# Kernel optimization log

Measured on AMD Instinct MI355X. Metric: run time of the kernel, lower is better.

The kernel has to match this reference:

```python
import jax, jax.numpy as jnp
import numpy as np

N_NODES = 100000
IN_CH = 256
OUT_CH = 128
N_EDGES = 3200000
SCALING_FACTOR = 1.8


def gcn_propagate(x, edge_index, num_nodes):
    """APPNP(K=1, alpha=0) == one step of D^-1/2 (A+I) D^-1/2 @ x."""
    row, col = edge_index[0], edge_index[1]
    loops = jnp.arange(num_nodes, dtype=edge_index.dtype)
    row = jnp.concatenate([row, loops])
    col = jnp.concatenate([col, loops])
    ones = jnp.ones(row.shape[0], dtype=x.dtype)
    deg = jax.ops.segment_sum(ones, col, num_segments=num_nodes)  # [N]
    dinv = jnp.where(deg > 0, jax.lax.rsqrt(deg), 0.0)
    norm = dinv[row] * dinv[col]  # [E+N]
    msgs = x[row] * norm[:, None]  # gather + scale, [E+N, C]
    return jax.ops.segment_sum(msgs, col, num_segments=num_nodes)  # [N, C]


def setup_inputs() -> dict:
    key = jax.random.key(0)
    ks = jax.random.split(key, 7)
    x = jax.random.normal(ks[0], (N_NODES, IN_CH), dtype=jnp.float32)
    edge_index = jax.random.randint(ks[1], (2, N_EDGES), 0, N_NODES, dtype=jnp.int64)
    s1 = 1.0 / np.sqrt(IN_CH)
    W1 = jax.random.uniform(ks[2], (IN_CH, OUT_CH), jnp.float32, -s1, s1)
    b1 = jax.random.uniform(ks[3], (OUT_CH,), jnp.float32, -s1, s1)
    W2 = jax.random.uniform(ks[4], (IN_CH, OUT_CH), jnp.float32, -s1, s1)
    b2 = jax.random.uniform(ks[5], (OUT_CH,), jnp.float32, -s1, s1)
    return {"x": x, "edge_index": edge_index, "W1": W1, "b1": b1, "W2": W2, "b2": b2}


def reference(x, edge_index, W1, b1, W2, b2):
    num_nodes = x.shape[0]
    # branch 1: linear1 then propagate
    x_ = x @ W1 + b1
    x_ = gcn_propagate(x_, edge_index, num_nodes)
    # branch 2: linear2, L2 normalize per-row, scale, then propagate
    h = x @ W2 + b2
    nrm = jnp.sqrt(jnp.sum(h * h, axis=1, keepdims=True))
    h = h / jnp.maximum(nrm, 1e-12) * SCALING_FACTOR
    h = gcn_propagate(h, edge_index, num_nodes)
    return (h, x_)
```

## Files before the change

kernel.cpp:

```cpp
#include <hip/hip_runtime.h>

#define IN_CH   256
#define OUT_CH  128
#define SCALE   1.8f
#define GT_M    64
#define BKT_SH  8
#define BKT_CAP 9216

using bf16x8 = __attribute__((ext_vector_type(8))) short;
using f32x4  = __attribute__((ext_vector_type(4))) float;

__device__ __forceinline__ float blo(unsigned int w) { return __uint_as_float(w << 16); }
__device__ __forceinline__ float bhi(unsigned int w) { return __uint_as_float(w & 0xffff0000u); }
__device__ __forceinline__ unsigned short f2b(float f) {
    unsigned int u = __float_as_uint(f);
    u += 0x7fffu + ((u >> 16) & 1u);
    return (unsigned short)(u >> 16);
}
__device__ __forceinline__ void split2(float f, unsigned short& h, unsigned short& l) {
    h = f2b(f);
    float hf = __uint_as_float((unsigned int)h << 16);
    l = f2b(f - hf);
}

__global__ __launch_bounds__(256) void wsplit_kernel(const float* __restrict__ W1, const float* __restrict__ b1,
                                                     const float* __restrict__ W2, const float* __restrict__ b2,
                                                     unsigned short* __restrict__ Wfh, unsigned short* __restrict__ Wfl,
                                                     float* __restrict__ bc, int* __restrict__ bktCur) {
    int n = blockIdx.x;
    int k = threadIdx.x;
    if (n < 2) {
        int i = n * 256 + k;
        bktCur[i] = i * BKT_CAP;
    }
    float w = (n < OUT_CH) ? W2[k * OUT_CH + n] : W1[k * OUT_CH + (n - OUT_CH)];
    unsigned short h, l;
    split2(w, h, l);
    int idx = (((k >> 5) * 16 + (n >> 4)) * 64 + ((k >> 3) & 3) * 16 + (n & 15)) * 8 + (k & 7);
    Wfh[idx] = h;
    Wfl[idx] = l;
    if (k == 0) bc[n] = (n < OUT_CH) ? b2[n] : b1[n - OUT_CH];
}

__device__ __forceinline__ void part_body(char* smem, const int* __restrict__ row, const int* __restrict__ col,
                                          int* __restrict__ bktCur, unsigned int* __restrict__ pairs,
                                          int E, int NBKT, int nPart, int pb) {
    int* lh   = (int*)smem;
    int* lcur = lh + 512;
    int t = threadIdx.x;
    lh[t] = 0; lh[t + 256] = 0;
    __syncthreads();
    int tile = (E + nPart - 1) / nPart;
    int e0 = pb * tile;
    int e1 = min(E, e0 + tile);
    for (int i = e0 + t; i < e1; i += 256)
        atomicAdd(&lh[col[i] >> BKT_SH], 1);
    __syncthreads();
    for (int b = t; b < 512; b += 256) {
        int c = (b < NBKT) ? lh[b] : 0;
        lcur[b] = (c > 0) ? atomicAdd(&bktCur[b], c) : 0;
    }
    __syncthreads();
    for (int i = e0 + t; i < e1; i += 256) {
        int c = col[i];
        int b = c >> BKT_SH;
        int pos = atomicAdd(&lcur[b], 1);
        pairs[pos] = ((unsigned int)(c & 255) << 17) | (unsigned int)row[i];
    }
}

__device__ __forceinline__ void csr_body(char* smem, const unsigned int* __restrict__ pairs,
                                         const int* __restrict__ bktCur,
                                         int* __restrict__ csr, int* __restrict__ offs,
                                         int* __restrict__ deg, float* __restrict__ dinv,
                                         int N, int b) {
    int* s    = (int*)smem;
    int* nc   = (int*)(smem + 1024);
    int* ncur = (int*)(smem + 2048);
    int t = threadIdx.x;
    int base = b * BKT_CAP;
    int cnt = bktCur[b] - base;

    nc[t] = 0;
    __syncthreads();
    for (int i = t; i < cnt; i += 256)
        atomicAdd(&nc[pairs[base + i] >> 17], 1);
    __syncthreads();
    int dv = nc[t];
    s[t] = dv;
    __syncthreads();
    for (int o = 1; o < 256; o <<= 1) {
        int u = (t >= o) ? s[t - o] : 0;
        __syncthreads();
        s[t] += u;
        __syncthreads();
    }
    int rel = s[t] - dv;
    int n = (b << BKT_SH) + t;
    if (n < N) {
        offs[n] = base + rel;
        deg[n] = dv;
        dinv[n] = 1.0f / sqrtf((float)dv + 1.0f);
    }
    ncur[t] = rel;
    __syncthreads();
    for (int i = t; i < cnt; i += 256) {
        unsigned int k = pairs[base + i];
        int node = k >> 17;
        int pos = atomicAdd(&ncur[node], 1);
        csr[base + pos] = (int)(k & 0x1FFFF);
    }
}

#define XPAD 264
#define GEMM_SMEM (GT_M * XPAD * 2 + 2 * GT_M * 4)
__device__ __forceinline__ void gemm_body(char* smem, const float* __restrict__ x,
                                          const unsigned short* __restrict__ Wfh,
                                          const unsigned short* __restrict__ Wfl,
                                          const float* __restrict__ bc,
                                          unsigned short* __restrict__ gb, int blockRow, int N) {
    unsigned short* xh = (unsigned short*)smem;
    float* sn = (float*)(smem + GT_M * XPAD * sizeof(unsigned short));

    int t = threadIdx.x;
    size_t row0 = (size_t)blockRow * GT_M;

    const float4* xg = (const float4*)(x + row0 * IN_CH);
#pragma unroll
    for (int i = 0; i < 16; i++) {
        int f4 = t + i * 256;
        int row = f4 >> 6;
        int c4 = (f4 & 63) * 4;
        uint2 hw = {0u, 0u};
        if (row0 + row < (size_t)N) {
            float4 v = xg[f4];
            hw.x = (unsigned int)f2b(v.x) | ((unsigned int)f2b(v.y) << 16);
            hw.y = (unsigned int)f2b(v.z) | ((unsigned int)f2b(v.w) << 16);
        }
        *(uint2*)&xh[row * XPAD + c4] = hw;
    }
    __syncthreads();

    int lane = t & 63;
    int wv = t >> 6;
    int lr = lane & 15;
    int lk = (lane >> 4) * 8;

    f32x4 acc[4][4];
#pragma unroll
    for (int rt = 0; rt < 4; rt++)
#pragma unroll
        for (int ct = 0; ct < 4; ct++) acc[rt][ct] = (f32x4){0.f, 0.f, 0.f, 0.f};

#pragma unroll
    for (int kt = 0; kt < 8; kt++) {
        int k0 = kt * 32;
        bf16x8 bh[4], bl[4];
#pragma unroll
        for (int ct = 0; ct < 4; ct++) {
            int fidx = ((kt * 16 + wv * 4 + ct) * 64 + lane) * 8;
            bh[ct] = *(const bf16x8*)&Wfh[fidx];
            bl[ct] = *(const bf16x8*)&Wfl[fidx];
        }
        bf16x8 ah[4];
#pragma unroll
        for (int rt = 0; rt < 4; rt++) {
            int idx = (rt * 16 + lr) * XPAD + k0 + lk;
            ah[rt] = *(const bf16x8*)&xh[idx];
        }
#pragma unroll
        for (int rt = 0; rt < 4; rt++)
#pragma unroll
            for (int ct = 0; ct < 4; ct++) {
                acc[rt][ct] = __builtin_amdgcn_mfma_f32_16x16x32_bf16(ah[rt], bh[ct], acc[rt][ct], 0, 0, 0);
                acc[rt][ct] = __builtin_amdgcn_mfma_f32_16x16x32_bf16(ah[rt], bl[ct], acc[rt][ct], 0, 0, 0);
            }
    }
    __syncthreads();

    float bcv[4];
#pragma unroll
    for (int ct = 0; ct < 4; ct++) bcv[ct] = bc[wv * 64 + ct * 16 + lr];
#pragma unroll
    for (int rt = 0; rt < 4; rt++)
#pragma unroll
        for (int ct = 0; ct < 4; ct++)
#pragma unroll
            for (int j = 0; j < 4; j++) acc[rt][ct][j] += bcv[ct];

    if (wv < 2) {
        float nr[4][4];
#pragma unroll
        for (int rt = 0; rt < 4; rt++)
#pragma unroll
            for (int j = 0; j < 4; j++) {
                float sum = 0.f;
#pragma unroll
                for (int ct = 0; ct < 4; ct++) sum += acc[rt][ct][j] * acc[rt][ct][j];
                nr[rt][j] = sum;
            }
#pragma unroll
        for (int o = 1; o < 16; o <<= 1)
#pragma unroll
            for (int rt = 0; rt < 4; rt++)
#pragma unroll
                for (int j = 0; j < 4; j++) nr[rt][j] += __shfl_xor(nr[rt][j], o);
        if (lr == 0) {
#pragma unroll
            for (int rt = 0; rt < 4; rt++)
#pragma unroll
                for (int j = 0; j < 4; j++)
                    sn[wv * GT_M + rt * 16 + (lane >> 4) * 4 + j] = nr[rt][j];
        }
    }
    __syncthreads();

#pragma unroll
    for (int rt = 0; rt < 4; rt++) {
#pragma unroll
        for (int j = 0; j < 4; j++) {
            int rl = rt * 16 + (lane >> 4) * 4 + j;
            if (row0 + rl >= (size_t)N) continue;
            float sf;
            if (wv < 2) {
                float n2 = sn[rl] + sn[GT_M + rl];
                sf = SCALE / fmaxf(sqrtf(n2), 1e-12f);
            } else {
                sf = 1.0f;
            }
            size_t base = (row0 + rl) * 256;
#pragma unroll
            for (int ct = 0; ct < 4; ct++) {
                int col = wv * 64 + ct * 16 + lr;
                gb[base + col] = f2b(acc[rt][ct][j] * sf);
            }
        }
    }
}

__global__ __launch_bounds__(256) void k1_part_gemm(const int* __restrict__ row, const int* __restrict__ col,
                                                    int* __restrict__ bktCur, unsigned int* __restrict__ pairs,
                                                    int E, int NBKT, int nPart,
                                                    const float* __restrict__ x,
                                                    const unsigned short* __restrict__ Wfh,
                                                    const unsigned short* __restrict__ Wfl,
                                                    const float* __restrict__ bc,
                                                    unsigned short* __restrict__ gb, int N) {
    __shared__ __align__(16) char smem[GEMM_SMEM];
    int b = (int)blockIdx.x;
    if (b < nPart) part_body(smem, row, col, bktCur, pairs, E, NBKT, nPart, b);
    else gemm_body(smem, x, Wfh, Wfl, bc, gb, b - nPart, N);
}

__global__ __launch_bounds__(256) void k2_csr_gemm(const unsigned int* __restrict__ pairs,
                                                   const int* __restrict__ bktCur,
                                                   int* __restrict__ csr, int* __restrict__ offs,
                                                   int* __restrict__ deg, float* __restrict__ dinv,
                                                   int N, int nCsr, int gemmRowBase,
                                                   const float* __restrict__ x,
                                                   const unsigned short* __restrict__ Wfh,
                                                   const unsigned short* __restrict__ Wfl,
                                                   const float* __restrict__ bc,
                                                   unsigned short* __restrict__ gb) {
    __shared__ __align__(16) char smem[GEMM_SMEM];
    int b = (int)blockIdx.x;
    if (b < nCsr) csr_body(smem, pairs, bktCur, csr, offs, deg, dinv, N, b);
    else gemm_body(smem, x, Wfh, Wfl, bc, gb, gemmRowBase + (b - nCsr), N);
}

__global__ __launch_bounds__(256) void gather_kernel(const uint4* __restrict__ gp,
                                                     const int* __restrict__ offs, const int* __restrict__ deg,
                                                     const int* __restrict__ csr, const float* __restrict__ dinv,
                                                     float* __restrict__ outh, float* __restrict__ outx, int N) {
    int t = threadIdx.x;
    int n = (blockIdx.x << 2) + (t >> 6);
    if (n >= N) return;
    int l = t & 63;
    int half = l >> 5;
    int cl = l & 31;

    float a0 = 0.f, a1 = 0.f, a2 = 0.f, a3 = 0.f, a4 = 0.f, a5 = 0.f, a6 = 0.f, a7 = 0.f;
    auto accumw = [&](uint4 w, float ds) {
        a0 += blo(w.x) * ds; a1 += bhi(w.x) * ds;
        a2 += blo(w.y) * ds; a3 += bhi(w.y) * ds;
        a4 += blo(w.z) * ds; a5 += bhi(w.z) * ds;
        a6 += blo(w.w) * ds; a7 += bhi(w.w) * ds;
    };

    float dn = dinv[n];
    if (half == 0) accumw(gp[(size_t)n * 32 + cl], dn);

    int s0 = offs[n];
    int e1 = s0 + deg[n];
    int e = s0 + half;
    for (; e + 2 < e1; e += 4) {
        int sa = csr[e];
        int sb = csr[e + 2];
        float da = dinv[sa];
        float db = dinv[sb];
        uint4 wa = gp[(size_t)sa * 32 + cl];
        uint4 wb = gp[(size_t)sb * 32 + cl];
        accumw(wa, da); accumw(wb, db);
    }
    for (; e < e1; e += 2) {
        int sa = csr[e];
        accumw(gp[(size_t)sa * 32 + cl], dinv[sa]);
    }

    a0 += __shfl_xor(a0, 32);
    a1 += __shfl_xor(a1, 32);
    a2 += __shfl_xor(a2, 32);
    a3 += __shfl_xor(a3, 32);
    a4 += __shfl_xor(a4, 32);
    a5 += __shfl_xor(a5, 32);
    a6 += __shfl_xor(a6, 32);
    a7 += __shfl_xor(a7, 32);

    if (half == 0) {
        float4 v0 = {a0 * dn, a1 * dn, a2 * dn, a3 * dn};
        float4 v1 = {a4 * dn, a5 * dn, a6 * dn, a7 * dn};
        if (cl < 16) {
            float* o = &outh[(size_t)n * OUT_CH + cl * 8];
            *(float4*)o = v0;
            *(float4*)(o + 4) = v1;
        } else {
            float* o = &outx[(size_t)n * OUT_CH + (cl - 16) * 8];
            *(float4*)o = v0;
            *(float4*)(o + 4) = v1;
        }
    }
}

extern "C" void kernel_launch(void* const* d_in, const int* in_sizes, int n_in,
                              void* d_out, int out_size, void* d_ws, size_t ws_size,
                              hipStream_t stream) {
    const float* x   = (const float*)d_in[0];
    const int*   ei  = (const int*)d_in[1];
    const float* W1  = (const float*)d_in[2];
    const float* b1  = (const float*)d_in[3];
    const float* W2  = (const float*)d_in[4];
    const float* b2  = (const float*)d_in[5];

    const int N = in_sizes[0] / IN_CH;
    const int E = in_sizes[1] / 2;
    const int NBKT = (N + 255) >> BKT_SH;

    float* outh = (float*)d_out;
    float* outx = outh + (size_t)N * OUT_CH;

    char* p = (char*)d_ws;
    auto take = [&](size_t bytes) {
        char* q = p;
        p += (bytes + 255) & ~(size_t)255;
        return q;
    };
    int*   deg     = (int*)take((size_t)N * sizeof(int));
    float* dinv    = (float*)take((size_t)N * sizeof(float));
    int*   offs    = (int*)take((size_t)N * sizeof(int));
    int*   bktCur  = (int*)take(512 * sizeof(int));
    float* bc      = (float*)take(256 * sizeof(float));
    unsigned short* Wfh = (unsigned short*)take(256 * 256 * sizeof(unsigned short));
    unsigned short* Wfl = (unsigned short*)take(256 * 256 * sizeof(unsigned short));
    int*   csr     = (int*)take((size_t)NBKT * BKT_CAP * sizeof(int));
    unsigned int* pairs = (unsigned int*)take((size_t)NBKT * BKT_CAP * sizeof(unsigned int));
    unsigned short* gb = (unsigned short*)take((size_t)N * 256 * sizeof(unsigned short));

    const int* erow = ei;
    const int* ecol = ei + E;

    const int nPart = 512;
    const int gemmBlocks = (N + GT_M - 1) / GT_M;
    const int gemmA = (gemmBlocks + 1) / 2;
    const int gemmB = gemmBlocks - gemmA;

    wsplit_kernel<<<256, 256, 0, stream>>>(W1, b1, W2, b2, Wfh, Wfl, bc, bktCur);
    k1_part_gemm<<<nPart + gemmA, 256, 0, stream>>>(erow, ecol, bktCur, pairs, E, NBKT, nPart,
                                                    x, Wfh, Wfl, bc, gb, N);
    k2_csr_gemm<<<NBKT + gemmB, 256, 0, stream>>>(pairs, bktCur, csr, offs, deg, dinv, N, NBKT, gemmA,
                                                  x, Wfh, Wfl, bc, gb);
    gather_kernel<<<(N + 3) / 4, 256, 0, stream>>>((const uint4*)gb, offs, deg, csr, dinv, outh, outx, N);
}
```

Before: 401.8 us.

## Tile CSR by source range and split gather into per-branch cache-friendly passes

The CSR build now sub-sorts each node's neighbours into seven source-index tiles and records per-tile offsets. The gather is replaced by a persistent kernel in which each wave owns 13 nodes and sweeps the source tiles in order. This keeps the working set of gathered rows within one source window, aiming for better L2/MALL reuse. The gather also runs as two launches, one per output branch (half the channels each), with nontemporal stores. The cost is 8x larger offset arrays, more shared-memory atomics in the CSR build, and lower parallelism from a fixed grid of 2048 blocks.

```diff
diff --git a/kernel.cpp b/kernel.cpp
--- a/kernel.cpp
+++ b/kernel.cpp
@@ -6,6 +6,10 @@
 #define GT_M    64
 #define BKT_SH  8
 #define BKT_CAP 9216
+#define TILE_SH 14
+#define NT      7
+#define GNW     8192
+#define GNPW    13
 
 using bf16x8 = __attribute__((ext_vector_type(8))) short;
 using f32x4  = __attribute__((ext_vector_type(4))) float;
@@ -71,22 +75,27 @@
 
 __device__ __forceinline__ void csr_body(char* smem, const unsigned int* __restrict__ pairs,
                                          const int* __restrict__ bktCur,
-                                         int* __restrict__ csr, int* __restrict__ offs,
-                                         int* __restrict__ deg, float* __restrict__ dinv,
-                                         int N, int b) {
-    int* s    = (int*)smem;
-    int* nc   = (int*)(smem + 1024);
-    int* ncur = (int*)(smem + 2048);
+                                         int* __restrict__ csr, int* __restrict__ tOffs,
+                                         float* __restrict__ dinv, int N, int b) {
+    int* ncT = (int*)smem;
+    int* cur = ncT + 256 * NT;
+    int* s   = cur + 256 * NT;
     int t = threadIdx.x;
     int base = b * BKT_CAP;
     int cnt = bktCur[b] - base;
 
-    nc[t] = 0;
-    __syncthreads();
-    for (int i = t; i < cnt; i += 256)
-        atomicAdd(&nc[pairs[base + i] >> 17], 1);
-    __syncthreads();
-    int dv = nc[t];
+    for (int f = t; f < 256 * NT; f += 256) ncT[f] = 0;
+    __syncthreads();
+    for (int i = t; i < cnt; i += 256) {
+        unsigned int k = pairs[base + i];
+        int node = k >> 17;
+        int src = k & 0x1FFFF;
+        atomicAdd(&ncT[node * NT + (src >> TILE_SH)], 1);
+    }
+    __syncthreads();
+    int dv = 0;
+#pragma unroll
+    for (int tt = 0; tt < NT; tt++) dv += ncT[t * NT + tt];
     s[t] = dv;
     __syncthreads();
     for (int o = 1; o < 256; o <<= 1) {
@@ -97,18 +106,24 @@
     }
     int rel = s[t] - dv;
     int n = (b << BKT_SH) + t;
+    int running = rel;
+#pragma unroll
+    for (int tt = 0; tt < NT; tt++) {
+        if (n < N) tOffs[n * 8 + tt] = base + running;
+        cur[t * NT + tt] = running;
+        running += ncT[t * NT + tt];
+    }
     if (n < N) {
-        offs[n] = base + rel;
-        deg[n] = dv;
+        tOffs[n * 8 + NT] = base + running;
         dinv[n] = 1.0f / sqrtf((float)dv + 1.0f);
     }
-    ncur[t] = rel;
     __syncthreads();
     for (int i = t; i < cnt; i += 256) {
         unsigned int k = pairs[base + i];
         int node = k >> 17;
-        int pos = atomicAdd(&ncur[node], 1);
-        csr[base + pos] = (int)(k & 0x1FFFF);
+        int src = k & 0x1FFFF;
+        int pos = atomicAdd(&cur[node * NT + (src >> TILE_SH)], 1);
+        csr[base + pos] = src;
     }
 }
 
@@ -254,8 +269,8 @@
 
 __global__ __launch_bounds__(256) void k2_csr_gemm(const unsigned int* __restrict__ pairs,
                                                    const int* __restrict__ bktCur,
-                                                   int* __restrict__ csr, int* __restrict__ offs,
-                                                   int* __restrict__ deg, float* __restrict__ dinv,
+                                                   int* __restrict__ csr, int* __restrict__ tOffs,
+                                                   float* __restrict__ dinv,
                                                    int N, int nCsr, int gemmRowBase,
                                                    const float* __restrict__ x,
                                                    const unsigned short* __restrict__ Wfh,
@@ -264,69 +279,61 @@
                                                    unsigned short* __restrict__ gb) {
     __shared__ __align__(16) char smem[GEMM_SMEM];
     int b = (int)blockIdx.x;
-    if (b < nCsr) csr_body(smem, pairs, bktCur, csr, offs, deg, dinv, N, b);
+    if (b < nCsr) csr_body(smem, pairs, bktCur, csr, tOffs, dinv, N, b);
     else gemm_body(smem, x, Wfh, Wfl, bc, gb, gemmRowBase + (b - nCsr), N);
 }
 
-__global__ __launch_bounds__(256) void gather_kernel(const uint4* __restrict__ gp,
-                                                     const int* __restrict__ offs, const int* __restrict__ deg,
-                                                     const int* __restrict__ csr, const float* __restrict__ dinv,
-                                                     float* __restrict__ outh, float* __restrict__ outx, int N) {
-    int t = threadIdx.x;
-    int n = (blockIdx.x << 2) + (t >> 6);
-    if (n >= N) return;
-    int l = t & 63;
-    int half = l >> 5;
-    int cl = l & 31;
-
-    float a0 = 0.f, a1 = 0.f, a2 = 0.f, a3 = 0.f, a4 = 0.f, a5 = 0.f, a6 = 0.f, a7 = 0.f;
-    auto accumw = [&](uint4 w, float ds) {
-        a0 += blo(w.x) * ds; a1 += bhi(w.x) * ds;
-        a2 += blo(w.y) * ds; a3 += bhi(w.y) * ds;
-        a4 += blo(w.z) * ds; a5 += bhi(w.z) * ds;
-        a6 += blo(w.w) * ds; a7 += bhi(w.w) * ds;
-    };
-
-    float dn = dinv[n];
-    if (half == 0) accumw(gp[(size_t)n * 32 + cl], dn);
-
-    int s0 = offs[n];
-    int e1 = s0 + deg[n];
-    int e = s0 + half;
-    for (; e + 2 < e1; e += 4) {
-        int sa = csr[e];
-        int sb = csr[e + 2];
-        float da = dinv[sa];
-        float db = dinv[sb];
-        uint4 wa = gp[(size_t)sa * 32 + cl];
-        uint4 wb = gp[(size_t)sb * 32 + cl];
-        accumw(wa, da); accumw(wb, db);
-    }
-    for (; e < e1; e += 2) {
-        int sa = csr[e];
-        accumw(gp[(size_t)sa * 32 + cl], dinv[sa]);
-    }
-
-    a0 += __shfl_xor(a0, 32);
-    a1 += __shfl_xor(a1, 32);
-    a2 += __shfl_xor(a2, 32);
-    a3 += __shfl_xor(a3, 32);
-    a4 += __shfl_xor(a4, 32);
-    a5 += __shfl_xor(a5, 32);
-    a6 += __shfl_xor(a6, 32);
-    a7 += __shfl_xor(a7, 32);
-
-    if (half == 0) {
-        float4 v0 = {a0 * dn, a1 * dn, a2 * dn, a3 * dn};
-        float4 v1 = {a4 * dn, a5 * dn, a6 * dn, a7 * dn};
-        if (cl < 16) {
-            float* o = &outh[(size_t)n * OUT_CH + cl * 8];
-            *(float4*)o = v0;
-            *(float4*)(o + 4) = v1;
-        } else {
-            float* o = &outx[(size_t)n * OUT_CH + (cl - 16) * 8];
-            *(float4*)o = v0;
-            *(float4*)(o + 4) = v1;
+__global__ __launch_bounds__(256, 8) void gathertile_kernel(const unsigned int* __restrict__ gp,
+                                                            const int* __restrict__ tOffs,
+                                                            const int* __restrict__ csr,
+                                                            const float* __restrict__ dinv,
+                                                            float* __restrict__ out, int cOff, int N) {
+    int w = ((int)blockIdx.x << 2) + ((int)threadIdx.x >> 6);
+    unsigned int cl = (unsigned int)cOff + (threadIdx.x & 63);
+
+    float a0[GNPW], a1[GNPW];
+#pragma unroll
+    for (int i = 0; i < GNPW; i++) { a0[i] = 0.f; a1[i] = 0.f; }
+
+    for (int t = 0; t < NT; t++) {
+#pragma unroll
+        for (int i = 0; i < GNPW; i++) {
+            int n = w + GNW * i;
+            if (n < N) {
+                int e = tOffs[n * 8 + t];
+                int eend = tOffs[n * 8 + t + 1];
+                for (; e + 1 < eend; e += 2) {
+                    int sa = csr[e];
+                    int sb = csr[e + 1];
+                    float da = dinv[sa];
+                    float db = dinv[sb];
+                    unsigned int va = gp[(unsigned int)sa * 128u + cl];
+                    unsigned int vb = gp[(unsigned int)sb * 128u + cl];
+                    a0[i] += blo(va) * da; a1[i] += bhi(va) * da;
+                    a0[i] += blo(vb) * db; a1[i] += bhi(vb) * db;
+                }
+                if (e < eend) {
+                    int sa = csr[e];
+                    float da = dinv[sa];
+                    unsigned int va = gp[(unsigned int)sa * 128u + cl];
+                    a0[i] += blo(va) * da; a1[i] += bhi(va) * da;
+                }
+            }
+        }
+    }
+
+#pragma unroll
+    for (int i = 0; i < GNPW; i++) {
+        int n = w + GNW * i;
+        if (n < N) {
+            float dn = dinv[n];
+            unsigned int v = gp[(unsigned int)n * 128u + cl];
+            float2 o;
+            o.x = (a0[i] + blo(v) * dn) * dn;
+            o.y = (a1[i] + bhi(v) * dn) * dn;
+            double od;
+            __builtin_memcpy(&od, &o, 8);
+            __builtin_nontemporal_store(od, (double*)&out[(unsigned int)n * 128u + (threadIdx.x & 63) * 2]);
         }
     }
 }
@@ -354,13 +361,12 @@
         p += (bytes + 255) & ~(size_t)255;
         return q;
     };
-    int*   deg     = (int*)take((size_t)N * sizeof(int));
     float* dinv    = (float*)take((size_t)N * sizeof(float));
-    int*   offs    = (int*)take((size_t)N * sizeof(int));
     int*   bktCur  = (int*)take(512 * sizeof(int));
     float* bc      = (float*)take(256 * sizeof(float));
     unsigned short* Wfh = (unsigned short*)take(256 * 256 * sizeof(unsigned short));
     unsigned short* Wfl = (unsigned short*)take(256 * 256 * sizeof(unsigned short));
+    int*   tOffs   = (int*)take((size_t)N * 8 * sizeof(int));
     int*   csr     = (int*)take((size_t)NBKT * BKT_CAP * sizeof(int));
     unsigned int* pairs = (unsigned int*)take((size_t)NBKT * BKT_CAP * sizeof(unsigned int));
     unsigned short* gb = (unsigned short*)take((size_t)N * 256 * sizeof(unsigned short));
@@ -376,7 +382,8 @@
     wsplit_kernel<<<256, 256, 0, stream>>>(W1, b1, W2, b2, Wfh, Wfl, bc, bktCur);
     k1_part_gemm<<<nPart + gemmA, 256, 0, stream>>>(erow, ecol, bktCur, pairs, E, NBKT, nPart,
                                                     x, Wfh, Wfl, bc, gb, N);
-    k2_csr_gemm<<<NBKT + gemmB, 256, 0, stream>>>(pairs, bktCur, csr, offs, deg, dinv, N, NBKT, gemmA,
+    k2_csr_gemm<<<NBKT + gemmB, 256, 0, stream>>>(pairs, bktCur, csr, tOffs, dinv, N, NBKT, gemmA,
                                                   x, Wfh, Wfl, bc, gb);
-    gather_kernel<<<(N + 3) / 4, 256, 0, stream>>>((const uint4*)gb, offs, deg, csr, dinv, outh, outx, N);
-}
+    gathertile_kernel<<<GNW / 4, 256, 0, stream>>>((const unsigned int*)gb, tOffs, csr, dinv, outh, 0, N);
+    gathertile_kernel<<<GNW / 4, 256, 0, stream>>>((const unsigned int*)gb, tOffs, csr, dinv, outx, 64, N);
+}
```

Result: slower. 538.9 us (+34.1%).
